# Kernel optimization log

Measured on AMD Instinct MI355X. Metric: run time of the kernel, lower is better.

## Reference

```python
import jax, jax.numpy as jnp
import numpy as np

B, IN, O = 256, 512, 10
STRUCTURES = list(range(32, 257, 32))  # 8 neuron structures
REPS, N_ACT = 4, 4


def _build_hidden_ids():
    ids = []
    i = 0
    # activation-major, then repetition, then structure (matches build_model_ids)
    for _ in range(N_ACT * REPS):
        for s in STRUCTURES:
            ids += [i] * s
            i += 1
    return np.asarray(ids, dtype=np.int32), i


def setup_inputs() -> dict:
    ids, M = _build_hidden_ids()
    H = len(ids)  # 18432
    k = jax.random.split(jax.random.key(0), 5)
    x = jax.random.normal(k[0], (B, IN), dtype=jnp.float32)
    hidden_w = jax.random.normal(k[1], (H, IN), dtype=jnp.float32) / np.sqrt(IN)
    hidden_b = jax.random.normal(k[2], (H,), dtype=jnp.float32) * 0.02
    out_w = jax.random.normal(k[3], (O, H), dtype=jnp.float32) * 0.05
    out_b = jax.random.normal(k[4], (M, O), dtype=jnp.float32) * 0.02
    return {"x": x, "hidden_w": hidden_w, "hidden_b": hidden_b,
            "out_w": out_w, "out_b": out_b,
            "hidden_ids": jnp.asarray(ids)}


_ACTS = [jax.nn.relu, jnp.tanh, jax.nn.sigmoid, lambda t: t]


def reference(x, hidden_w, hidden_b, out_w, out_b, hidden_ids):
    # hidden layer: [B, H]
    h = x @ hidden_w.T + hidden_b
    # per-activation contiguous splits (equal size H // n_act)
    chunks = jnp.split(h, N_ACT, axis=1)
    a = jnp.concatenate([f(c) for f, c in zip(_ACTS, chunks)], axis=1)  # [B, H]
    # per-hidden-neuron contribution to each output unit: [B, H, O]
    contrib = a[:, :, None] * out_w.T[None, :, :]
    M = out_b.shape[0]
    # segment-reduce hidden neurons into their model id: [M, B, O] -> [B, M, O]
    agg = jax.ops.segment_sum(contrib.transpose(1, 0, 2), hidden_ids, num_segments=M)
    return agg.transpose(1, 0, 2) + out_b[None, :, :]
```

## Files before the change

### kernel.cpp

```cpp
#include <hip/hip_runtime.h>
#include <hip/hip_bf16.h>

typedef __bf16 bf16x8 __attribute__((ext_vector_type(8)));
typedef float floatx4 __attribute__((ext_vector_type(4)));

#define BATCH 256
#define INDIM 512
#define ODIM 10
#define HTOT 18432
#define NMODEL 128
#define HTILE 64
#define BTILE 64
#define BK 64
#define LSTRIDE 72
#define ACT_CHUNK 4608
#define NJPG (HTOT / 32)

__device__ __forceinline__ unsigned pk2(float a, float b) {
    unsigned ua = __float_as_uint(a);
    ua = (ua + 0x7fffu + ((ua >> 16) & 1u)) >> 16;
    unsigned ub = __float_as_uint(b);
    ub = (ub + 0x7fffu + ((ub >> 16) & 1u)) >> 16;
    return ua | (ub << 16);
}

__device__ __forceinline__ float apply_act(float h, int aidx) {
    if (aidx == 0) return fmaxf(h, 0.f);
    if (aidx == 1) return 1.f - 2.f / (1.f + __expf(2.f * h));
    if (aidx == 2) return 1.f / (1.f + __expf(-h));
    return h;
}

__global__ __launch_bounds__(256, 4) void mlp_kernel(
    const float* __restrict__ x, const float* __restrict__ hidden_w,
    const float* __restrict__ hidden_b, const float* __restrict__ out_w,
    float* __restrict__ ws)
{
    __shared__ unsigned short xs[BTILE * LSTRIDE];
    __shared__ unsigned short wsx[HTILE * LSTRIDE];
    __shared__ float wtile[ODIM * HTILE];
    __shared__ float btile[HTILE];

    const int tid = threadIdx.x;
    const int bid = blockIdx.x;
    const int jb = bid >> 2, bb = bid & 3;
    const int j0 = jb * HTILE;
    const int b0 = bb * BTILE;
    const int lane = tid & 63;
    const int wvid = tid >> 6;
    const int r = lane & 15;
    const int g = lane >> 4;

    for (int i = tid; i < ODIM * HTILE; i += 256)
        wtile[i] = out_w[(i >> 6) * HTOT + j0 + (i & 63)];
    if (tid < HTILE) btile[tid] = hidden_b[j0 + tid];

    floatx4 acc[4];
    #pragma unroll
    for (int jt = 0; jt < 4; jt++) acc[jt] = (floatx4)0.f;

    const floatx4* xv  = (const floatx4*)x;
    const floatx4* wv4 = (const floatx4*)hidden_w;

    for (int kk = 0; kk < INDIM; kk += BK) {
        const int kq = kk >> 2;
        #pragma unroll
        for (int i = 0; i < 4; i++) {
            int f = tid + i * 256;
            int row = f >> 4, c4 = f & 15;
            floatx4 v = xv[(size_t)(b0 + row) * (INDIM / 4) + kq + c4];
            floatx4 u = wv4[(size_t)(j0 + row) * (INDIM / 4) + kq + c4];
            *(uint2*)&xs[row * LSTRIDE + c4 * 4]  = make_uint2(pk2(v[0], v[1]), pk2(v[2], v[3]));
            *(uint2*)&wsx[row * LSTRIDE + c4 * 4] = make_uint2(pk2(u[0], u[1]), pk2(u[2], u[3]));
        }
        __syncthreads();

        #pragma unroll
        for (int s = 0; s < 2; s++) {
            bf16x8 bfr = *(const bf16x8*)&xs[(wvid * 16 + r) * LSTRIDE + s * 32 + g * 8];
            #pragma unroll
            for (int jt = 0; jt < 4; jt++) {
                bf16x8 af = *(const bf16x8*)&wsx[(jt * 16 + r) * LSTRIDE + s * 32 + g * 8];
                acc[jt] = __builtin_amdgcn_mfma_f32_16x16x32_bf16(af, bfr, acc[jt], 0, 0, 0);
            }
        }
        __syncthreads();
    }

    const int aidx = j0 / ACT_CHUNK;
    const int b = b0 + wvid * 16 + r;

    #pragma unroll
    for (int jp = 0; jp < 2; jp++) {
        const int jpg = (j0 >> 5) + jp;
        float a[2][4];
        #pragma unroll
        for (int h = 0; h < 2; h++) {
            int jt = jp * 2 + h;
            #pragma unroll
            for (int q = 0; q < 4; q++)
                a[h][q] = apply_act(acc[jt][q] + btile[jt * 16 + g * 4 + q], aidx);
        }
        #pragma unroll
        for (int o = 0; o < ODIM; o++) {
            float p = 0.f;
            #pragma unroll
            for (int h = 0; h < 2; h++) {
                int jt = jp * 2 + h;
                const float* wr = &wtile[o * HTILE + jt * 16 + g * 4];
                p += a[h][0] * wr[0] + a[h][1] * wr[1] + a[h][2] * wr[2] + a[h][3] * wr[3];
            }
            p += __shfl_xor(p, 16, 64);
            p += __shfl_xor(p, 32, 64);
            if (lane < 16)
                ws[((size_t)jpg * ODIM + o) * BATCH + b] = p;
        }
    }
}

__global__ __launch_bounds__(256) void finalize_kernel(
    const float* __restrict__ ws, const float* __restrict__ out_b,
    float* __restrict__ out)
{
    const int mo = blockIdx.x;
    const int m = mo / ODIM, o = mo - m * ODIM;
    const int b = threadIdx.x;
    const int rep = m >> 3, idx = m & 7;
    const int jp0 = rep * 36 + (idx * (idx + 1)) / 2;
    const int cnt = idx + 1;

    float s = out_b[mo];
    for (int c = 0; c < cnt; c++)
        s += ws[((size_t)(jp0 + c) * ODIM + o) * BATCH + b];
    out[((size_t)b * NMODEL + m) * ODIM + o] = s;
}

extern "C" void kernel_launch(void* const* d_in, const int* in_sizes, int n_in,
                              void* d_out, int out_size, void* d_ws, size_t ws_size,
                              hipStream_t stream) {
    const float* x   = (const float*)d_in[0];
    const float* hw  = (const float*)d_in[1];
    const float* hb  = (const float*)d_in[2];
    const float* ow  = (const float*)d_in[3];
    const float* ob  = (const float*)d_in[4];
    float* out = (float*)d_out;
    float* ws  = (float*)d_ws;

    mlp_kernel<<<(HTOT / HTILE) * (BATCH / BTILE), 256, 0, stream>>>(x, hw, hb, ow, ws);
    finalize_kernel<<<NMODEL * ODIM, 256, 0, stream>>>(ws, ob, out);
}
```

Baseline: 115.1 us.

## Prefetch next K-slice into registers and remap blocks for XCD locality

Loads the next K-slice of x and hidden_w into registers while the current slice is processed with MFMA, overlapping global memory latency with compute. Also remaps block indices so the four batch-tile blocks sharing a weight tile, and contiguous weight tiles, land on the same XCD, improving L2 reuse of hidden_w. The prefetch costs extra registers, which may pressure occupancy.

Result: faster. 111.8 us (-2.9%).

```diff
diff --git a/kernel.cpp b/kernel.cpp
--- a/kernel.cpp
+++ b/kernel.cpp
@@ -43,7 +43,9 @@
 
     const int tid = threadIdx.x;
     const int bid = blockIdx.x;
-    const int jb = bid >> 2, bb = bid & 3;
+    const int r8 = bid & 7, t = bid >> 3;
+    const int jb = r8 * 36 + (t >> 2);
+    const int bb = t & 3;
     const int j0 = jb * HTILE;
     const int b0 = bb * BTILE;
     const int lane = tid & 63;
@@ -62,18 +64,35 @@
     const floatx4* xv  = (const floatx4*)x;
     const floatx4* wv4 = (const floatx4*)hidden_w;
 
+    const int f_row[4] = { (tid + 0)   >> 4, (tid + 256) >> 4,
+                           (tid + 512) >> 4, (tid + 768) >> 4 };
+    const int f_c4 = tid & 15;
+
+    floatx4 vx[4], vw[4];
+    #pragma unroll
+    for (int i = 0; i < 4; i++) {
+        vx[i] = xv[(size_t)(b0 + f_row[i]) * (INDIM / 4) + f_c4];
+        vw[i] = wv4[(size_t)(j0 + f_row[i]) * (INDIM / 4) + f_c4];
+    }
+
     for (int kk = 0; kk < INDIM; kk += BK) {
-        const int kq = kk >> 2;
         #pragma unroll
         for (int i = 0; i < 4; i++) {
-            int f = tid + i * 256;
-            int row = f >> 4, c4 = f & 15;
-            floatx4 v = xv[(size_t)(b0 + row) * (INDIM / 4) + kq + c4];
-            floatx4 u = wv4[(size_t)(j0 + row) * (INDIM / 4) + kq + c4];
-            *(uint2*)&xs[row * LSTRIDE + c4 * 4]  = make_uint2(pk2(v[0], v[1]), pk2(v[2], v[3]));
-            *(uint2*)&wsx[row * LSTRIDE + c4 * 4] = make_uint2(pk2(u[0], u[1]), pk2(u[2], u[3]));
+            *(uint2*)&xs[f_row[i] * LSTRIDE + f_c4 * 4]  =
+                make_uint2(pk2(vx[i][0], vx[i][1]), pk2(vx[i][2], vx[i][3]));
+            *(uint2*)&wsx[f_row[i] * LSTRIDE + f_c4 * 4] =
+                make_uint2(pk2(vw[i][0], vw[i][1]), pk2(vw[i][2], vw[i][3]));
         }
         __syncthreads();
+
+        if (kk + BK < INDIM) {
+            const int kq = (kk + BK) >> 2;
+            #pragma unroll
+            for (int i = 0; i < 4; i++) {
+                vx[i] = xv[(size_t)(b0 + f_row[i]) * (INDIM / 4) + kq + f_c4];
+                vw[i] = wv4[(size_t)(j0 + f_row[i]) * (INDIM / 4) + kq + f_c4];
+            }
+        }
 
         #pragma unroll
         for (int s = 0; s < 2; s++) {
```
